# Optimization experiments

Hardware: AMD Instinct MI355X
Metric: run time of the kernel (lower is better)

## Reference

```python
import jax, jax.numpy as jnp
import numpy as np

RATIO = 10.0
MAXPOOL_K = 101   # local-max window (samples)
MED_K = 6000      # MAD window (samples)
MED_STRIDE = MED_K // 2
TOP_K = 100


def setup_inputs() -> dict:
    key = jax.random.key(0)
    xcorr = jax.random.normal(key, (2, 3, 16, 360000), dtype=jnp.float32)
    return {"xcorr": xcorr}


def _detect(xcorr):
    nb, nc, nx, nt = xcorr.shape
    neg = jnp.finfo(xcorr.dtype).min
    # max_pool2d kernel (1, 101), stride 1, pad (0, 50) -> local sliding max over time
    smax = jax.lax.reduce_window(
        xcorr, neg, jax.lax.max,
        (1, 1, 1, MAXPOOL_K), (1, 1, 1, 1),
        [(0, 0), (0, 0), (0, 0), (MAXPOOL_K // 2, MAXPOOL_K // 2)])
    # reflect-pad right by MED_K then unfold(size=MED_K, stride=MED_STRIDE)
    padded = jnp.pad(xcorr, ((0, 0), (0, 0), (0, 0), (0, MED_K)), mode='reflect')
    nblocks = (nt + MED_K) // MED_STRIDE  # exact by construction
    blocks = padded.reshape(nb, nc, nx, nblocks, MED_STRIDE)
    # each window = two consecutive half-overlapping blocks -> [nb,nc,nx,nw,MED_K]
    windows = jnp.concatenate([blocks[..., :-1, :], blocks[..., 1:, :]], axis=-1)
    mid = (MED_K - 1) // 2  # torch.median returns lower median for even n
    med = jnp.sort(windows, axis=-1)[..., mid]
    mad = jnp.sort(jnp.abs(windows - med[..., None]), axis=-1)[..., mid]  # [nb,nc,nx,nw]
    # bilinear interpolate along time by scale MED_STRIDE (align_corners=False), crop to nt
    in_w = mad.shape[-1]
    pos = (jnp.arange(nt, dtype=jnp.float32) + 0.5) / MED_STRIDE - 0.5
    pos = jnp.maximum(pos, 0.0)
    x0 = jnp.minimum(jnp.floor(pos).astype(jnp.int32), in_w - 1)
    x1 = jnp.minimum(x0 + 1, in_w - 1)
    w = pos - x0.astype(jnp.float32)
    mad_t = mad[..., x0] * (1.0 - w) + mad[..., x1] * w  # [nb,nc,nx,nt]
    # keep local maxima exceeding ratio * MAD, zero the rest, then top-k per trace
    keep = (smax == xcorr) & (xcorr > RATIO * mad_t)
    masked = xcorr * keep.astype(xcorr.dtype)
    topk_scores, topk_inds = jax.lax.top_k(masked, TOP_K)
    return topk_scores, topk_inds


def reference(xcorr):
    return _detect(xcorr)
```

## Files before the change

### kernel.cpp

```cpp
#include <hip/hip_runtime.h>
#include <stdint.h>

#define NT      360000
#define NTRACE  96
#define MEDK    6000
#define MSTRIDE 3000
#define NW      121
#define HALFW   50
#define TOPK    100
#define DETCAP  128
#define RATIO_F 10.0f
#define DCHUNKS 24
#define CAP     2304
#define NCOPY   8
#define HSTRIDE 257
#define NSLOT   6

__device__ __forceinline__ uint32_t f2key(float f) {
    uint32_t u = __float_as_uint(f);
    return u ^ (uint32_t)(((int32_t)u >> 31) | 0x80000000);
}
__device__ __forceinline__ float key2f(uint32_t k) {
    uint32_t u = (k & 0x80000000u) ? (k & 0x7fffffffu) : ~k;
    return __uint_as_float(u);
}

struct SelShared {
    uint32_t hist[NCOPY * HSTRIDE];
    uint32_t cmp[CAP];
    uint32_t segtot[4];
    uint32_t s_bin, s_rank, s_cnt, ccount;
};

__device__ void bin_select(SelShared* sh, uint32_t rank)
{
    const int tid  = threadIdx.x;
    const int lane = tid & 63;
    const int wv   = tid >> 6;
    uint32_t c = 0;
    #pragma unroll
    for (int j = 0; j < NCOPY; ++j) c += sh->hist[j * HSTRIDE + tid];
    uint32_t incl = c;
    #pragma unroll
    for (int off = 1; off < 64; off <<= 1) {
        uint32_t v = __shfl_up(incl, off);
        if (lane >= off) incl += v;
    }
    if (lane == 63) sh->segtot[wv] = incl;
    __syncthreads();
    uint32_t segoff = 0;
    for (int j = 0; j < wv; ++j) segoff += sh->segtot[j];
    incl += segoff;
    uint32_t excl = incl - c;
    if (rank > excl && rank <= incl) {
        sh->s_bin = (uint32_t)tid; sh->s_rank = rank - excl; sh->s_cnt = c;
    }
    __syncthreads();
}

__device__ __forceinline__ void zero_hist(SelShared* sh)
{
    uint4* h4 = (uint4*)sh->hist;
    for (int i = threadIdx.x; i < 514; i += 256) h4[i] = make_uint4(0, 0, 0, 0);
}

__device__ float select_from_regs(const float4 (&r)[NSLOT], float sub, bool useabs,
                                  SelShared* sh)
{
    const int tid  = threadIdx.x;
    const int lane = tid & 63;
    uint32_t* myhist = &sh->hist[(tid >> 5) * HSTRIDE];

    zero_hist(sh);
    if (tid == 0) sh->ccount = 0;
    __syncthreads();
    #pragma unroll
    for (int k = 0; k < NSLOT; ++k) {
        if (k * 256 + tid < MEDK / 4) {
            float vv[4] = {r[k].x, r[k].y, r[k].z, r[k].w};
            #pragma unroll
            for (int e = 0; e < 4; ++e) {
                float v = vv[e];
                if (useabs) v = fabsf(v - sub);
                atomicAdd(&myhist[f2key(v) >> 24], 1u);
            }
        }
    }
    __syncthreads();
    bin_select(sh, 3000u);
    const uint32_t b0 = sh->s_bin, cnt = sh->s_cnt;
    uint32_t rank   = sh->s_rank;
    uint32_t prefix = b0 << 24;
    uint32_t pmask  = 0xFF000000u;
    const bool usec = (cnt <= CAP);

    if (usec) {
        #pragma unroll
        for (int k = 0; k < NSLOT; ++k) {
            bool valid = (k * 256 + tid < MEDK / 4);
            float vv[4] = {r[k].x, r[k].y, r[k].z, r[k].w};
            #pragma unroll
            for (int e = 0; e < 4; ++e) {
                uint32_t key = 0; bool m = false;
                if (valid) {
                    float v = vv[e];
                    if (useabs) v = fabsf(v - sub);
                    key = f2key(v);
                    m = ((key >> 24) == b0);
                }
                unsigned long long b = __ballot(m);
                if (b) {
                    int leader = __ffsll((unsigned long long)b) - 1;
                    uint32_t pcnt = (uint32_t)__popcll(b & ((1ull << lane) - 1ull));
                    uint32_t wbase = 0;
                    if (lane == leader) wbase = atomicAdd(&sh->ccount, (uint32_t)__popcll(b));
                    wbase = __shfl(wbase, leader);
                    if (m) sh->cmp[wbase + pcnt] = key;
                }
            }
        }
        __syncthreads();
    }

    for (int pass = 1; pass < 4; ++pass) {
        const int shift = 24 - 8 * pass;
        zero_hist(sh);
        __syncthreads();
        if (usec) {
            for (int i = tid; i < (int)cnt; i += 256) {
                uint32_t k = sh->cmp[i];
                if ((k & pmask) == prefix)
                    atomicAdd(&myhist[(k >> shift) & 0xFFu], 1u);
            }
        } else {
            #pragma unroll
            for (int k = 0; k < NSLOT; ++k) {
                if (k * 256 + tid < MEDK / 4) {
                    float vv[4] = {r[k].x, r[k].y, r[k].z, r[k].w};
                    #pragma unroll
                    for (int e = 0; e < 4; ++e) {
                        float v = vv[e];
                        if (useabs) v = fabsf(v - sub);
                        uint32_t kk = f2key(v);
                        if ((kk & pmask) == prefix)
                            atomicAdd(&myhist[(kk >> shift) & 0xFFu], 1u);
                    }
                }
            }
        }
        __syncthreads();
        bin_select(sh, rank);
        prefix |= sh->s_bin << shift;
        pmask  |= 0xFFu << shift;
        rank    = sh->s_rank;
        __syncthreads();
    }
    return key2f(prefix);
}

__global__ __launch_bounds__(256, 5) void mad_kernel(const float* __restrict__ x,
                                                     float* __restrict__ mad)
{
    __shared__ SelShared sh;
    const int tr = blockIdx.x / NW;
    const int w  = blockIdx.x % NW;
    const float* xt = x + (size_t)tr * NT;
    const int t0 = w * MSTRIDE;

    float4 r[NSLOT];
    if (t0 + MEDK <= NT) {
        const float4* src4 = (const float4*)(xt + t0);
        #pragma unroll
        for (int k = 0; k < NSLOT; ++k) {
            int i4 = k * 256 + threadIdx.x;
            r[k] = (i4 < MEDK / 4) ? src4[i4] : make_float4(0.f, 0.f, 0.f, 0.f);
        }
    } else {
        #pragma unroll
        for (int k = 0; k < NSLOT; ++k) {
            int i4 = k * 256 + threadIdx.x;
            float tmp[4] = {0.f, 0.f, 0.f, 0.f};
            if (i4 < MEDK / 4) {
                #pragma unroll
                for (int e = 0; e < 4; ++e) {
                    int g = t0 + i4 * 4 + e;
                    int src = (g < NT) ? g : (2 * NT - 2 - g);
                    tmp[e] = xt[src];
                }
            }
            r[k] = make_float4(tmp[0], tmp[1], tmp[2], tmp[3]);
        }
    }
    __syncthreads();
    float med  = select_from_regs(r, 0.0f, false, &sh);
    __syncthreads();
    float madv = select_from_regs(r, med,  true,  &sh);
    if (threadIdx.x == 0) mad[tr * NW + w] = madv;
}

__global__ __launch_bounds__(256) void detect_kernel(const float* __restrict__ x,
                                                     const float* __restrict__ mad,
                                                     uint32_t* __restrict__ counters,
                                                     uint64_t* __restrict__ det)
{
    __shared__ float smad[NW];
    const int tr = blockIdx.x / DCHUNKS;
    const int ch = blockIdx.x % DCHUNKS;
    const float* xt = x + (size_t)tr * NT;
    for (int i = threadIdx.x; i < NW; i += 256) smad[i] = mad[tr * NW + i];
    __syncthreads();
    const int tbeg = ch * (NT / DCHUNKS);
    const int tend = tbeg + (NT / DCHUNKS);
    const int stride = 256 * 4;
    int t0 = tbeg + threadIdx.x * 4;
    float4 nxt = (t0 < tend) ? *(const float4*)(xt + t0)
                             : make_float4(0.f, 0.f, 0.f, 0.f);
    for (int t = t0; t < tend; t += stride) {
        float4 v4 = nxt;
        int tn = t + stride;
        if (tn < tend) nxt = *(const float4*)(xt + tn);
        float vv[4] = {v4.x, v4.y, v4.z, v4.w};
        #pragma unroll
        for (int k = 0; k < 4; ++k) {
            int   tt = t + k;
            float v  = vv[k];
            float pos = ((float)tt + 0.5f) / (float)MSTRIDE - 0.5f;
            pos = fmaxf(pos, 0.0f);
            int   x0 = min((int)floorf(pos), NW - 1);
            int   x1 = min(x0 + 1, NW - 1);
            float wg = pos - (float)x0;
            float m  = smad[x0] * (1.0f - wg) + smad[x1] * wg;
            if (v > RATIO_F * m) {
                bool ismax = true;
                int lo = max(tt - HALFW, 0), hi = min(tt + HALFW, NT - 1);
                for (int j = lo; j <= hi && ismax; ++j) ismax = (xt[j] <= v);
                if (ismax) {
                    uint32_t slot = atomicAdd(&counters[tr], 1u);
                    if (slot < DETCAP)
                        det[(size_t)tr * DETCAP + slot] =
                            ((uint64_t)f2key(v) << 32) | (uint32_t)(~(uint32_t)tt);
                }
            }
        }
    }
}

__global__ __launch_bounds__(64) void finalize_kernel(const float* __restrict__ x,
                                                      const uint32_t* __restrict__ counters,
                                                      const uint64_t* __restrict__ det,
                                                      float* __restrict__ out)
{
    __shared__ uint64_t sdet[DETCAP];
    __shared__ int sposs[TOPK];
    __shared__ int snegs[TOPK];
    __shared__ int s_np, s_nn;
    const int tr   = blockIdx.x;
    const int lane = threadIdx.x;
    const int D = (int)min(counters[tr], (uint32_t)DETCAP);
    for (int i = lane; i < D; i += 64) sdet[i] = det[(size_t)tr * DETCAP + i];
    if (lane == 0) { s_np = 0; s_nn = 0; }
    __syncthreads();

    const float* xt = x + (size_t)tr * NT;
    for (int base = 0; base < NT; base += 64) {
        int np0 = s_np, nn0 = s_nn;
        if (np0 >= TOPK && nn0 >= TOPK) break;
        int  t     = base + lane;
        bool valid = (t < NT);
        uint32_t bits = valid ? __float_as_uint(xt[t]) : 0u;
        bool nonneg = valid && !(bits >> 31);
        bool neg    = valid &&  (bits >> 31);
        if (nonneg && D > 0) {
            for (int i = 0; i < D; ++i) {
                int dt = (int)(~(uint32_t)(sdet[i] & 0xFFFFFFFFull));
                if (dt == t) { nonneg = false; break; }
            }
        }
        unsigned long long bp = __ballot(nonneg);
        unsigned long long bn = __ballot(neg);
        unsigned long long below = (1ull << lane) - 1ull;
        int pidx = np0 + __popcll(bp & below);
        int nidx = nn0 + __popcll(bn & below);
        if (nonneg && pidx < TOPK) sposs[pidx] = t;
        if (neg    && nidx < TOPK) snegs[nidx] = t;
        __syncthreads();
        if (lane == 0) { s_np = np0 + __popcll(bp); s_nn = nn0 + __popcll(bn); }
        __syncthreads();
    }
    __syncthreads();

    if (lane == 0) {
        for (int i = 1; i < D; ++i) {
            uint64_t k = sdet[i]; int j = i - 1;
            while (j >= 0 && sdet[j] < k) { sdet[j + 1] = sdet[j]; --j; }
            sdet[j + 1] = k;
        }
    }
    __syncthreads();

    const int nd   = min(D, TOPK);
    const int npos = min(s_np, TOPK);
    float* oscore = out + (size_t)tr * TOPK;
    float* oidx   = out + (size_t)NTRACE * TOPK + (size_t)tr * TOPK;
    for (int j = lane; j < TOPK; j += 64) {
        float sc; int idx;
        if (j < nd) {
            uint64_t k = sdet[j];
            sc  = key2f((uint32_t)(k >> 32));
            idx = (int)(~(uint32_t)(k & 0xFFFFFFFFull));
        } else if (j - nd < npos) {
            sc = 0.0f;  idx = sposs[j - nd];
        } else {
            int jj = j - nd - npos;
            sc = -0.0f; idx = (jj < TOPK) ? snegs[jj] : 0;
        }
        oscore[j] = sc;
        oidx[j]   = (float)idx;
    }
}

extern "C" void kernel_launch(void* const* d_in, const int* in_sizes, int n_in,
                              void* d_out, int out_size, void* d_ws, size_t ws_size,
                              hipStream_t stream)
{
    const float* x = (const float*)d_in[0];
    float* out = (float*)d_out;
    char* ws = (char*)d_ws;
    float*    mad      = (float*)ws;
    uint32_t* counters = (uint32_t*)(ws + 46464);
    uint64_t* det      = (uint64_t*)(ws + 46464 + 384);

    hipMemsetAsync(counters, 0, NTRACE * sizeof(uint32_t), stream);
    hipLaunchKernelGGL(mad_kernel,    dim3(NTRACE * NW),      dim3(256), 0, stream, x, mad);
    hipLaunchKernelGGL(detect_kernel, dim3(NTRACE * DCHUNKS), dim3(256), 0, stream, x, mad, counters, det);
    hipLaunchKernelGGL(finalize_kernel, dim3(NTRACE),         dim3(64),  0, stream, x, counters, det, out);
}
```

Before: 493.2 us.

## Compute each MAD window's median selection in a single wavefront instead of a block

Each median/MAD window is now handled by one 64-lane wavefront instead of a 256-thread block, with four windows per block. The radix select uses 9-bit first-pass histograms. All __syncthreads barriers and shared-counter atomics in the selection are replaced by wave-local LDS waits and ballot-based compaction. Each lane now holds 24 float4 registers, which raises register pressure and lowers the occupancy bound from 5 to 3. The fallback path for an oversized candidate bin re-reads global memory.

```diff
diff --git a/kernel.cpp b/kernel.cpp
--- a/kernel.cpp
+++ b/kernel.cpp
@@ -11,10 +11,11 @@
 #define DETCAP  128
 #define RATIO_F 10.0f
 #define DCHUNKS 24
-#define CAP     2304
-#define NCOPY   8
-#define HSTRIDE 257
-#define NSLOT   6
+#define WPB     4
+#define NSLOT   24
+#define NF4     1500
+#define HWORDS  1026
+#define CMPCAP  2048
 
 __device__ __forceinline__ uint32_t f2key(float f) {
     uint32_t u = __float_as_uint(f);
@@ -25,177 +26,178 @@
     return __uint_as_float(u);
 }
 
-struct SelShared {
-    uint32_t hist[NCOPY * HSTRIDE];
-    uint32_t cmp[CAP];
-    uint32_t segtot[4];
-    uint32_t s_bin, s_rank, s_cnt, ccount;
-};
-
-__device__ void bin_select(SelShared* sh, uint32_t rank)
-{
-    const int tid  = threadIdx.x;
-    const int lane = tid & 63;
-    const int wv   = tid >> 6;
-    uint32_t c = 0;
-    #pragma unroll
-    for (int j = 0; j < NCOPY; ++j) c += sh->hist[j * HSTRIDE + tid];
-    uint32_t incl = c;
+__device__ __forceinline__ void wsync() {
+    asm volatile("s_waitcnt lgkmcnt(0)" ::: "memory");
+}
+
+__device__ __forceinline__ void wbin_select512(const uint32_t* whist, int lane,
+                                               uint32_t rank, uint32_t& bin,
+                                               uint32_t& subrank, uint32_t& cnt)
+{
+    uint32_t c[8], s[8];
+    #pragma unroll
+    for (int j = 0; j < 8; ++j) {
+        int b = j * 64 + lane;
+        c[j] = whist[b] + whist[513 + b];
+        s[j] = c[j];
+    }
     #pragma unroll
     for (int off = 1; off < 64; off <<= 1) {
-        uint32_t v = __shfl_up(incl, off);
-        if (lane >= off) incl += v;
-    }
-    if (lane == 63) sh->segtot[wv] = incl;
-    __syncthreads();
-    uint32_t segoff = 0;
-    for (int j = 0; j < wv; ++j) segoff += sh->segtot[j];
-    incl += segoff;
-    uint32_t excl = incl - c;
-    if (rank > excl && rank <= incl) {
-        sh->s_bin = (uint32_t)tid; sh->s_rank = rank - excl; sh->s_cnt = c;
-    }
-    __syncthreads();
-}
-
-__device__ __forceinline__ void zero_hist(SelShared* sh)
-{
-    uint4* h4 = (uint4*)sh->hist;
-    for (int i = threadIdx.x; i < 514; i += 256) h4[i] = make_uint4(0, 0, 0, 0);
-}
-
-__device__ float select_from_regs(const float4 (&r)[NSLOT], float sub, bool useabs,
-                                  SelShared* sh)
-{
-    const int tid  = threadIdx.x;
-    const int lane = tid & 63;
-    uint32_t* myhist = &sh->hist[(tid >> 5) * HSTRIDE];
-
-    zero_hist(sh);
-    if (tid == 0) sh->ccount = 0;
-    __syncthreads();
+        #pragma unroll
+        for (int j = 0; j < 8; ++j) {
+            uint32_t t = __shfl_up(s[j], off);
+            if (lane >= off) s[j] += t;
+        }
+    }
+    uint32_t base = 0, fb = 0, fr = 0, fc = 0;
+    bool found = false;
+    #pragma unroll
+    for (int j = 0; j < 8; ++j) {
+        uint32_t T    = __shfl(s[j], 63);
+        uint32_t incl = base + s[j];
+        uint32_t excl = incl - c[j];
+        if (rank > excl && rank <= incl) {
+            found = true; fb = (uint32_t)(j * 64 + lane); fr = rank - excl; fc = c[j];
+        }
+        base += T;
+    }
+    unsigned long long bal = __ballot(found);
+    int src = __ffsll(bal) - 1;
+    bin     = __shfl(fb, src);
+    subrank = __shfl(fr, src);
+    cnt     = __shfl(fc, src);
+}
+
+template<bool ABS>
+__device__ float wave_select(const float4 (&r)[NSLOT], int lane, float sub,
+                             uint32_t* whist, uint32_t* wcmp,
+                             const float* xt, int t0)
+{
+    uint32_t* myh = whist + (lane >> 5) * 513;
+
+    for (int i = lane; i < HWORDS; i += 64) whist[i] = 0;
+    wsync();
     #pragma unroll
     for (int k = 0; k < NSLOT; ++k) {
-        if (k * 256 + tid < MEDK / 4) {
+        if (k < 23 || lane < 28) {
             float vv[4] = {r[k].x, r[k].y, r[k].z, r[k].w};
             #pragma unroll
             for (int e = 0; e < 4; ++e) {
                 float v = vv[e];
-                if (useabs) v = fabsf(v - sub);
-                atomicAdd(&myhist[f2key(v) >> 24], 1u);
-            }
-        }
-    }
-    __syncthreads();
-    bin_select(sh, 3000u);
-    const uint32_t b0 = sh->s_bin, cnt = sh->s_cnt;
-    uint32_t rank   = sh->s_rank;
-    uint32_t prefix = b0 << 24;
-    uint32_t pmask  = 0xFF000000u;
-    const bool usec = (cnt <= CAP);
+                if (ABS) v = fabsf(v - sub);
+                atomicAdd(&myh[f2key(v) >> 23], 1u);
+            }
+        }
+    }
+    wsync();
+    uint32_t bin, rank, cnt;
+    wbin_select512(whist, lane, 3000u, bin, rank, cnt);
+    uint32_t prefix = bin << 23;
+    uint32_t pmask  = 0xFF800000u;
+    const bool usec = (cnt <= CMPCAP);
 
     if (usec) {
+        uint32_t woff = 0;
+        const unsigned long long below = (1ull << lane) - 1ull;
         #pragma unroll
         for (int k = 0; k < NSLOT; ++k) {
-            bool valid = (k * 256 + tid < MEDK / 4);
             float vv[4] = {r[k].x, r[k].y, r[k].z, r[k].w};
             #pragma unroll
             for (int e = 0; e < 4; ++e) {
+                bool valid = (k < 23 || lane < 28);
                 uint32_t key = 0; bool m = false;
                 if (valid) {
                     float v = vv[e];
-                    if (useabs) v = fabsf(v - sub);
+                    if (ABS) v = fabsf(v - sub);
                     key = f2key(v);
-                    m = ((key >> 24) == b0);
+                    m = ((key >> 23) == bin);
                 }
-                unsigned long long b = __ballot(m);
-                if (b) {
-                    int leader = __ffsll((unsigned long long)b) - 1;
-                    uint32_t pcnt = (uint32_t)__popcll(b & ((1ull << lane) - 1ull));
-                    uint32_t wbase = 0;
-                    if (lane == leader) wbase = atomicAdd(&sh->ccount, (uint32_t)__popcll(b));
-                    wbase = __shfl(wbase, leader);
-                    if (m) sh->cmp[wbase + pcnt] = key;
-                }
-            }
-        }
-        __syncthreads();
-    }
-
+                unsigned long long bal = __ballot(m);
+                if (m) wcmp[woff + (uint32_t)__popcll(bal & below)] = key;
+                woff += (uint32_t)__popcll(bal);
+            }
+        }
+        wsync();
+    }
+
+    #pragma unroll
     for (int pass = 1; pass < 4; ++pass) {
-        const int shift = 24 - 8 * pass;
-        zero_hist(sh);
-        __syncthreads();
+        const int      shift = (pass == 1) ? 15 : (pass == 2) ? 7 : 0;
+        const uint32_t bm    = (pass == 3) ? 0x7Fu : 0xFFu;
+        for (int i = lane; i < HWORDS; i += 64) whist[i] = 0;
+        wsync();
         if (usec) {
-            for (int i = tid; i < (int)cnt; i += 256) {
-                uint32_t k = sh->cmp[i];
-                if ((k & pmask) == prefix)
-                    atomicAdd(&myhist[(k >> shift) & 0xFFu], 1u);
+            const int n = (int)cnt;
+            for (int i = lane; i < n; i += 64) {
+                uint32_t key = wcmp[i];
+                if ((key & pmask) == prefix)
+                    atomicAdd(&myh[(key >> shift) & bm], 1u);
             }
         } else {
-            #pragma unroll
-            for (int k = 0; k < NSLOT; ++k) {
-                if (k * 256 + tid < MEDK / 4) {
-                    float vv[4] = {r[k].x, r[k].y, r[k].z, r[k].w};
-                    #pragma unroll
-                    for (int e = 0; e < 4; ++e) {
-                        float v = vv[e];
-                        if (useabs) v = fabsf(v - sub);
-                        uint32_t kk = f2key(v);
-                        if ((kk & pmask) == prefix)
-                            atomicAdd(&myhist[(kk >> shift) & 0xFFu], 1u);
-                    }
-                }
-            }
-        }
-        __syncthreads();
-        bin_select(sh, rank);
-        prefix |= sh->s_bin << shift;
-        pmask  |= 0xFFu << shift;
-        rank    = sh->s_rank;
-        __syncthreads();
+            for (int i = lane; i < MEDK; i += 64) {
+                int g  = t0 + i;
+                int sg = (g < NT) ? g : (2 * NT - 2 - g);
+                float v = xt[sg];
+                if (ABS) v = fabsf(v - sub);
+                uint32_t key = f2key(v);
+                if ((key & pmask) == prefix)
+                    atomicAdd(&myh[(key >> shift) & bm], 1u);
+            }
+        }
+        wsync();
+        uint32_t b2, r2, c2;
+        wbin_select512(whist, lane, rank, b2, r2, c2);
+        prefix |= b2 << shift;
+        pmask  |= bm << shift;
+        rank    = r2;
+        wsync();
     }
     return key2f(prefix);
 }
 
-__global__ __launch_bounds__(256, 5) void mad_kernel(const float* __restrict__ x,
+__global__ __launch_bounds__(256, 3) void mad_kernel(const float* __restrict__ x,
                                                      float* __restrict__ mad)
 {
-    __shared__ SelShared sh;
-    const int tr = blockIdx.x / NW;
-    const int w  = blockIdx.x % NW;
+    __shared__ uint32_t hist_s[WPB * HWORDS];
+    __shared__ uint32_t cmp_s[WPB * CMPCAP];
+    const int wv   = threadIdx.x >> 6;
+    const int lane = threadIdx.x & 63;
+    const int wid  = blockIdx.x * WPB + wv;
+    const int tr   = wid / NW;
+    const int wi   = wid % NW;
     const float* xt = x + (size_t)tr * NT;
-    const int t0 = w * MSTRIDE;
+    const int t0 = wi * MSTRIDE;
 
     float4 r[NSLOT];
     if (t0 + MEDK <= NT) {
         const float4* src4 = (const float4*)(xt + t0);
         #pragma unroll
         for (int k = 0; k < NSLOT; ++k) {
-            int i4 = k * 256 + threadIdx.x;
-            r[k] = (i4 < MEDK / 4) ? src4[i4] : make_float4(0.f, 0.f, 0.f, 0.f);
+            int i4 = k * 64 + lane;
+            r[k] = (i4 < NF4) ? src4[i4] : make_float4(0.f, 0.f, 0.f, 0.f);
         }
     } else {
         #pragma unroll
         for (int k = 0; k < NSLOT; ++k) {
-            int i4 = k * 256 + threadIdx.x;
+            int i4 = k * 64 + lane;
             float tmp[4] = {0.f, 0.f, 0.f, 0.f};
-            if (i4 < MEDK / 4) {
+            if (i4 < NF4) {
                 #pragma unroll
                 for (int e = 0; e < 4; ++e) {
-                    int g = t0 + i4 * 4 + e;
-                    int src = (g < NT) ? g : (2 * NT - 2 - g);
-                    tmp[e] = xt[src];
+                    int g  = t0 + i4 * 4 + e;
+                    int sg = (g < NT) ? g : (2 * NT - 2 - g);
+                    tmp[e] = xt[sg];
                 }
             }
             r[k] = make_float4(tmp[0], tmp[1], tmp[2], tmp[3]);
         }
     }
-    __syncthreads();
-    float med  = select_from_regs(r, 0.0f, false, &sh);
-    __syncthreads();
-    float madv = select_from_regs(r, med,  true,  &sh);
-    if (threadIdx.x == 0) mad[tr * NW + w] = madv;
+
+    uint32_t* whist = hist_s + wv * HWORDS;
+    uint32_t* wcmp  = cmp_s  + wv * CMPCAP;
+    float med  = wave_select<false>(r, lane, 0.0f, whist, wcmp, xt, t0);
+    float madv = wave_select<true >(r, lane, med,  whist, wcmp, xt, t0);
+    if (lane == 0) mad[wid] = madv;
 }
 
 __global__ __launch_bounds__(256) void detect_kernel(const float* __restrict__ x,
@@ -331,7 +333,7 @@
     uint64_t* det      = (uint64_t*)(ws + 46464 + 384);
 
     hipMemsetAsync(counters, 0, NTRACE * sizeof(uint32_t), stream);
-    hipLaunchKernelGGL(mad_kernel,    dim3(NTRACE * NW),      dim3(256), 0, stream, x, mad);
+    hipLaunchKernelGGL(mad_kernel, dim3(NTRACE * NW / WPB), dim3(256), 0, stream, x, mad);
     hipLaunchKernelGGL(detect_kernel, dim3(NTRACE * DCHUNKS), dim3(256), 0, stream, x, mad, counters, det);
     hipLaunchKernelGGL(finalize_kernel, dim3(NTRACE),         dim3(64),  0, stream, x, counters, det, out);
 }
```

Result: slower. 513.8 us (+4.2%).
